# Optimization experiments

Hardware: AMD Instinct MI355X
Metric: run time of the kernel (lower is better)

The kernel has to match this reference:

```python
import jax, jax.numpy as jnp
import numpy as np

B, N, D = 2, 2048, 1024
H = 16                      # num_heads, head_dim = 64
E, K, CF = 4, 2, 1.0        # num_experts, top_k, capacity_factor
MLP_H = int(D * 4.0)        # dense Mlp hidden (mlp_ratio=4.0)
MOE_H = int(D * 0.25)       # expert hidden (hard-coded dim*0.25 in source)


def setup_inputs() -> dict:
    key = jax.random.key(0)
    ks = jax.random.split(key, 12)
    r = lambda k, shp, s=0.02: jax.random.normal(k, shp, jnp.float32) * s
    return dict(
        x=jax.random.normal(ks[0], (B, N, D), jnp.float32),
        noise=jax.random.normal(ks[1], (B, N, E), jnp.float32),
        ln1_g=jnp.ones((D,), jnp.float32), ln1_b=jnp.zeros((D,), jnp.float32),
        ln2_g=jnp.ones((D,), jnp.float32), ln2_b=jnp.zeros((D,), jnp.float32),
        w_qkv=r(ks[2], (3 * D, D)),
        w_proj=r(ks[3], (D, D)), b_proj=jnp.zeros((D,), jnp.float32),
        w_route=r(ks[4], (D, E), 0.05), b_route=jnp.zeros((E,), jnp.float32),
        w_noise=r(ks[5], (D, E), 0.05), b_noise=jnp.zeros((E,), jnp.float32),
        we1=r(ks[6], (E, D, MOE_H)), be1=jnp.zeros((E, MOE_H), jnp.float32),
        we2=r(ks[7], (E, MOE_H, D)), be2=jnp.zeros((E, D), jnp.float32),
        w_mlp1=r(ks[8], (D, MLP_H)), b_mlp1=jnp.zeros((MLP_H,), jnp.float32),
        w_mlp2=r(ks[9], (MLP_H, D)), b_mlp2=jnp.zeros((D,), jnp.float32),
    )


def _ln(x, g, b, eps=1e-5):
    mu = x.mean(-1, keepdims=True)
    var = ((x - mu) ** 2).mean(-1, keepdims=True)
    return (x - mu) * jax.lax.rsqrt(var + eps) * g + b


def _gelu(x):
    return jax.nn.gelu(x, approximate=False)  # torch nn.GELU default (erf)


def reference(x, noise, ln1_g, ln1_b, ln2_g, ln2_b, w_qkv, w_proj, b_proj,
              w_route, b_route, w_noise, b_noise, we1, be1, we2, be2,
              w_mlp1, b_mlp1, w_mlp2, b_mlp2):
    Bs, Ns, Ds = x.shape
    hd = Ds // H
    # --- attention branch ---
    x1 = _ln(x, ln1_g, ln1_b)
    qkv = (x1 @ w_qkv.T).reshape(Bs, Ns, 3, H, hd).transpose(2, 0, 3, 1, 4)
    q, k, v = qkv[0] * (hd ** -0.5), qkv[1], qkv[2]
    attn = jax.nn.softmax(jnp.einsum('bhnd,bhmd->bhnm', q, k), axis=-1)
    ao = jnp.einsum('bhnm,bhmd->bhnd', attn, v).transpose(0, 2, 1, 3).reshape(Bs, Ns, Ds)
    x = x + (ao @ w_proj.T + b_proj)
    # --- shared norm for mlp + moe ---
    x2 = _ln(x, ln2_g, ln2_b)
    # --- noisy top-k router ---
    logits = x2 @ w_route + b_route                  # [B,N,E]
    noisy = logits + noise * jax.nn.softplus(x2 @ w_noise + b_noise)
    topv, topi = jax.lax.top_k(noisy, K)             # [B,N,K]
    probs = jax.nn.softmax(topv, axis=-1)            # softmax over sparse logits == softmax over top-k
    T = Bs * Ns
    flat_x = x2.reshape(T, Ds)
    fidx = topi.reshape(T, K)
    rows = jnp.arange(T)[:, None]
    gate = jnp.zeros((T, E), noisy.dtype).at[rows, fidx].set(probs.reshape(T, K))
    capacity = int(T * K / E * CF)
    # --- capacity-limited dispatch / expert MLP / combine ---
    def dispatch(eid, W1, b1, W2, b2):
        mask = jnp.any(fidx == eid, axis=-1)                     # [T]
        order = jnp.argsort(jnp.logical_not(mask))               # stable: selected tokens first, in token order
        sel = order[:capacity]                                   # [C]
        valid = mask[sel].astype(flat_x.dtype)
        h = _gelu(flat_x[sel] @ W1 + b1)
        out = h @ W2 + b2
        w = gate[sel, eid] * valid
        return sel, out * w[:, None]
    sel, outw = jax.vmap(dispatch)(jnp.arange(E), we1, be1, we2, be2)   # [E,C], [E,C,D]
    moe = jnp.zeros_like(flat_x).at[sel.reshape(-1)].add(outw.reshape(-1, Ds)).reshape(Bs, Ns, Ds)
    # --- dense mlp branch ---
    mlp = _gelu(x2 @ w_mlp1 + b_mlp1) @ w_mlp2 + b_mlp2
    return x + mlp + moe
```

## Files before the change

### kernel.cpp

```cpp
#include <hip/hip_runtime.h>
#include <hip/hip_bf16.h>
#include <math.h>

typedef __bf16 bf16;
typedef __bf16 bf16x4 __attribute__((ext_vector_type(4)));
typedef __bf16 bf16x8 __attribute__((ext_vector_type(8)));
typedef float  f32x4  __attribute__((ext_vector_type(4)));

#define T_TOK 4096
#define DIM   1024
#define NHEAD 16
#define SEQ   2048
#define NEXP  4
#define CAP   2048
#define MLPH  4096
#define MOEH  256

__device__ __forceinline__ float gelu_exact(float v) {
    return 0.5f * v * (1.f + erff(v * 0.70710678118654752f));
}

struct HL { bf16 h, l; };
__device__ __forceinline__ HL split2(float v) {
    HL r; r.h = (bf16)v; r.l = (bf16)(v - (float)r.h); return r;
}

__device__ __forceinline__ float fast_exp2(float x) {
#if __has_builtin(__builtin_amdgcn_exp2f)
    return __builtin_amdgcn_exp2f(x);
#else
    return exp2f(x);
#endif
}

__device__ __forceinline__ void gload16(const bf16* gptr, bf16* lptr) {
    __builtin_amdgcn_global_load_lds(
        (const __attribute__((address_space(1))) unsigned int*)gptr,
        (__attribute__((address_space(3))) unsigned int*)lptr,
        16, 0, 0);
}

__device__ __forceinline__ bf16x8 sw_frag(const bf16* arr, int row, int cc) {
    return *(const bf16x8*)&arr[row * 64 + ((cc ^ (row & 7)) * 8)];
}

__global__ __launch_bounds__(256)
void ln_split_kernel(const float* __restrict__ x, const float* __restrict__ g,
                     const float* __restrict__ b, bf16* __restrict__ oh, bf16* __restrict__ ol) {
    int wave = threadIdx.x >> 6, lane = threadIdx.x & 63;
    long t = (long)blockIdx.x * 4 + wave;
    const float* xr = x + t * DIM;
    float v[16];
    #pragma unroll
    for (int i = 0; i < 16; i++) v[i] = xr[i * 64 + lane];
    float s = 0.f, s2 = 0.f;
    #pragma unroll
    for (int i = 0; i < 16; i++) { s += v[i]; s2 += v[i] * v[i]; }
    #pragma unroll
    for (int m = 1; m < 64; m <<= 1) { s += __shfl_xor(s, m); s2 += __shfl_xor(s2, m); }
    float mu  = s * (1.f / DIM);
    float var = s2 * (1.f / DIM) - mu * mu;
    float rs  = 1.f / sqrtf(var + 1e-5f);
    #pragma unroll
    for (int i = 0; i < 16; i++) {
        int d = i * 64 + lane;
        HL sp = split2((v[i] - mu) * rs * g[d] + b[d]);
        oh[t * DIM + d] = sp.h; ol[t * DIM + d] = sp.l;
    }
}

__global__ __launch_bounds__(256)
void split_pair_kernel(const float* __restrict__ in, bf16* __restrict__ h, bf16* __restrict__ l) {
    long i0 = ((long)blockIdx.x * 256 + threadIdx.x) * 4;
    f32x4 v = *(const f32x4*)&in[i0];
    bf16x4 vh, vl;
    #pragma unroll
    for (int j = 0; j < 4; j++) { HL sp = split2(v[j]); vh[j] = sp.h; vl[j] = sp.l; }
    *(bf16x4*)&h[i0] = vh; *(bf16x4*)&l[i0] = vl;
}

__global__ __launch_bounds__(256)
void transpose_conv_kernel(const float* __restrict__ in, bf16* __restrict__ out, int R, int C) {
    __shared__ bf16 tile[32][33];
    long bo = (long)blockIdx.z * R * C;
    in += bo; out += bo;
    int c0 = blockIdx.x * 32, r0 = blockIdx.y * 32;
    int tx = threadIdx.x & 31, ty = threadIdx.x >> 5;
    #pragma unroll
    for (int i = 0; i < 32; i += 8)
        tile[ty + i][tx] = (bf16)in[(long)(r0 + ty + i) * C + c0 + tx];
    __syncthreads();
    #pragma unroll
    for (int i = 0; i < 32; i += 8)
        out[(long)(c0 + ty + i) * R + r0 + tx] = tile[tx][ty + i];
}

__global__ __launch_bounds__(256)
void gemm_qkv(const bf16* __restrict__ Ah_g, const bf16* __restrict__ Al_g,
              const bf16* __restrict__ Bh_g, const bf16* __restrict__ Bl_g,
              bf16* __restrict__ Qh_g, bf16* __restrict__ Ql_g,
              bf16* __restrict__ Kh_g, bf16* __restrict__ Kl_g,
              bf16* __restrict__ VtI) {
    const int K = DIM;
    __shared__ alignas(16) bf16 Ah[8192], Al[8192], Bh[8192], Bl[8192];
    int tid = threadIdx.x;
    int wave = tid >> 6, lane = tid & 63;
    int l16 = lane & 15, l4 = lane >> 4;
    int wr = (wave >> 1) * 64, wc = (wave & 1) * 64;
    int row0 = blockIdx.y * 128, col0 = blockIdx.x * 128;
    int r8s = lane >> 3;
    int colb = ((lane & 7) ^ r8s) * 8;
    f32x4 acc[4][4] = {};
    for (int k0 = 0; k0 < K; k0 += 64) {
        #pragma unroll
        for (int p = 0; p < 4; p++) {
            int rl = p * 32 + wave * 8 + r8s;
            int lb = p * 2048 + wave * 512;
            gload16(&Ah_g[(long)(row0 + rl) * K + k0 + colb], &Ah[lb]);
            gload16(&Al_g[(long)(row0 + rl) * K + k0 + colb], &Al[lb]);
            gload16(&Bh_g[(long)(col0 + rl) * K + k0 + colb], &Bh[lb]);
            gload16(&Bl_g[(long)(col0 + rl) * K + k0 + colb], &Bl[lb]);
        }
        __syncthreads();
        #pragma unroll
        for (int ks = 0; ks < 2; ks++) {
            bf16x8 ah[4], al[4], bh[4], bl[4];
            #pragma unroll
            for (int i = 0; i < 4; i++) {
                ah[i] = sw_frag(Ah, wr + i*16 + l16, ks*4 + l4);
                al[i] = sw_frag(Al, wr + i*16 + l16, ks*4 + l4);
            }
            #pragma unroll
            for (int j = 0; j < 4; j++) {
                bh[j] = sw_frag(Bh, wc + j*16 + l16, ks*4 + l4);
                bl[j] = sw_frag(Bl, wc + j*16 + l16, ks*4 + l4);
            }
            #pragma unroll
            for (int i = 0; i < 4; i++)
                #pragma unroll
                for (int j = 0; j < 4; j++) {
                    acc[i][j] = __builtin_amdgcn_mfma_f32_16x16x32_bf16(ah[i], bh[j], acc[i][j], 0, 0, 0);
                    acc[i][j] = __builtin_amdgcn_mfma_f32_16x16x32_bf16(ah[i], bl[j], acc[i][j], 0, 0, 0);
                    acc[i][j] = __builtin_amdgcn_mfma_f32_16x16x32_bf16(al[i], bh[j], acc[i][j], 0, 0, 0);
                }
        }
        __syncthreads();
    }
    if (col0 < 2048) {
        bool isQ = (col0 < 1024);
        bf16* oh = isQ ? Qh_g : Kh_g;
        bf16* ol = isQ ? Ql_g : Kl_g;
        float qscale = isQ ? 0.18033688011112043f : 1.0f;
        #pragma unroll
        for (int i = 0; i < 4; i++)
            #pragma unroll
            for (int r = 0; r < 4; r++) {
                int t = row0 + wr + i * 16 + l4 * 4 + r;
                int bq = t >> 11, s = t & 2047;
                #pragma unroll
                for (int j = 0; j < 4; j++) {
                    int col = (col0 + wc + j * 16 + l16) & 1023;
                    int hh = col >> 6, dl = col & 63;
                    long o = ((long)(bq * NHEAD + hh) * SEQ + s) * 64 + dl;
                    HL sp = split2(acc[i][j][r] * qscale);
                    oh[o] = sp.h;
                    if (!isQ) ol[o] = sp.l;
                }
            }
    } else {
        #pragma unroll
        for (int i = 0; i < 4; i++) {
            int s0 = row0 + wr + i * 16 + l4 * 4;
            int b = s0 >> 11, sl = s0 & 2047;
            #pragma unroll
            for (int j = 0; j < 4; j++) {
                int d = col0 - 2048 + wc + j * 16 + l16;
                int h = d >> 6, dl = d & 63;
                long base = ((long)(b * NHEAD + h) * 64 + dl) * (2 * SEQ) + 2 * sl;
                bf16x8 vi;
                #pragma unroll
                for (int r = 0; r < 4; r++) {
                    HL sp = split2(acc[i][j][r]);
                    vi[2 * r] = sp.h; vi[2 * r + 1] = sp.l;
                }
                *(bf16x8*)&VtI[base] = vi;
            }
        }
    }
}

__global__ __launch_bounds__(512, 4)
void flash_attn(const bf16* __restrict__ Qh_g,
                const bf16* __restrict__ Kh_g, const bf16* __restrict__ Kl_g,
                const bf16* __restrict__ VtI_g,
                bf16* __restrict__ aoh, bf16* __restrict__ aol) {
    __shared__ alignas(16) bf16 KhS[2][4096], KlS[2][4096], VIS[2][8192];
    int tid = threadIdx.x;
    int wave = tid >> 6, lane = tid & 63;
    int l16 = lane & 15, l4 = lane >> 4;
    int bid = blockIdx.x;
    int bh = bid & 31;
    int b = bh >> 4, h = bh & 15;
    int q0 = (bid >> 5) * 128;

    bf16x8 qfh[2];
    {
        const bf16* qh = Qh_g + ((long)bh * SEQ + q0 + wave * 16 + l16) * 64;
        #pragma unroll
        for (int ks = 0; ks < 2; ks++)
            qfh[ks] = *(const bf16x8*)&qh[ks * 32 + l4 * 8];
    }
    int r8 = lane >> 3;
    int c8 = lane & 7;
    int r4 = lane >> 4, c16 = lane & 15;
    const bf16* kh_g = Kh_g + (long)bh * SEQ * 64;
    const bf16* kl_g = Kl_g + (long)bh * SEQ * 64;
    const bf16* vI_g = VtI_g + (long)bh * 64 * (2 * SEQ);

    float m_s = -1e30f, l_s = 0.f;
    f32x4 accO[4] = {};

    auto stage = [&](int c0, int bsel) {
        int R0 = wave * 8;
        int row = R0 + r8;
        int ksw = (c8 ^ r8) * 8;
        gload16(&kh_g[(long)(c0 + row) * 64 + ksw], &KhS[bsel][R0 * 64]);
        gload16(&kl_g[(long)(c0 + row) * 64 + ksw], &KlS[bsel][R0 * 64]);
        #pragma unroll
        for (int q = 0; q < 2; q++) {
            int d0 = R0 + q * 4 + r4;
            gload16(&vI_g[(long)d0 * (2 * SEQ) + 2 * c0 + ((c16 ^ (d0 & 15)) * 8)],
                    &VIS[bsel][(R0 + q * 4) * 128]);
        }
    };

    auto compute = [&](const bf16* KhT, const bf16* KlT, const bf16* VIT) {
        f32x4 st[4] = {};
        __builtin_amdgcn_s_setprio(1);
        #pragma unroll
        for (int ks = 0; ks < 2; ks++) {
            #pragma unroll
            for (int i = 0; i < 4; i++) {
                bf16x8 akh = sw_frag(KhT, i * 16 + l16, ks * 4 + l4);
                bf16x8 akl = sw_frag(KlT, i * 16 + l16, ks * 4 + l4);
                st[i] = __builtin_amdgcn_mfma_f32_16x16x32_bf16(akh, qfh[ks], st[i], 0, 0, 0);
                st[i] = __builtin_amdgcn_mfma_f32_16x16x32_bf16(akl, qfh[ks], st[i], 0, 0, 0);
            }
        }
        __builtin_amdgcn_s_setprio(0);
        float mx = st[0][0];
        #pragma unroll
        for (int i = 0; i < 4; i++)
            #pragma unroll
            for (int r = 0; r < 4; r++) mx = fmaxf(mx, st[i][r]);
        mx = fmaxf(mx, __shfl_xor(mx, 16));
        mx = fmaxf(mx, __shfl_xor(mx, 32));
        if (!__all(mx <= m_s + 8.f)) {
            float mnew = fmaxf(m_s, mx);
            float alpha = fast_exp2(m_s - mnew);
            l_s *= alpha;
            #pragma unroll
            for (int i = 0; i < 4; i++)
                #pragma unroll
                for (int r = 0; r < 4; r++) accO[i][r] *= alpha;
            m_s = mnew;
        }
        float psum = 0.f;
        bf16x8 pw[4];
        #pragma unroll
        for (int kb = 0; kb < 4; kb++)
            #pragma unroll
            for (int r = 0; r < 4; r++) {
                float pv = fast_exp2(st[kb][r] - m_s);
                psum += pv;
                bf16 pb = (bf16)pv;
                pw[kb][2 * r] = pb; pw[kb][2 * r + 1] = pb;
            }
        psum += __shfl_xor(psum, 16);
        psum += __shfl_xor(psum, 32);
        l_s += psum;
        __builtin_amdgcn_s_setprio(1);
        #pragma unroll
        for (int kb = 0; kb < 4; kb++) {
            #pragma unroll
            for (int i = 0; i < 4; i++) {
                int d = i * 16 + l16;
                bf16x8 av = *(const bf16x8*)&VIT[d * 128 + (((kb * 4 + l4) ^ (d & 15)) * 8)];
                accO[i] = __builtin_amdgcn_mfma_f32_16x16x32_bf16(av, pw[kb], accO[i], 0, 0, 0);
            }
        }
        __builtin_amdgcn_s_setprio(0);
    };

    const int NT = SEQ / 64;
    stage(0, 0);
    #pragma unroll 1
    for (int t = 0; t < NT; t += 2) {
        stage((t + 1) * 64, 1);
        asm volatile("s_waitcnt vmcnt(4)" ::: "memory");
        __builtin_amdgcn_sched_barrier(0);
        __builtin_amdgcn_s_barrier();
        compute(KhS[0], KlS[0], VIS[0]);
        asm volatile("" ::: "memory");
        __builtin_amdgcn_s_barrier();
        if (t + 2 < NT) {
            stage((t + 2) * 64, 0);
            asm volatile("s_waitcnt vmcnt(4)" ::: "memory");
        } else {
            asm volatile("s_waitcnt vmcnt(0)" ::: "memory");
        }
        __builtin_amdgcn_sched_barrier(0);
        __builtin_amdgcn_s_barrier();
        compute(KhS[1], KlS[1], VIS[1]);
        asm volatile("" ::: "memory");
        __builtin_amdgcn_s_barrier();
    }

    float inv = 1.f / l_s;
    int q = q0 + wave * 16 + l16;
    #pragma unroll
    for (int i = 0; i < 4; i++) {
        bf16x4 oh4, ol4;
        #pragma unroll
        for (int r = 0; r < 4; r++) { HL sp = split2(accO[i][r] * inv); oh4[r] = sp.h; ol4[r] = sp.l; }
        long o = ((long)(b * SEQ + q)) * DIM + h * 64 + i * 16 + l4 * 4;
        *(bf16x4*)&aoh[o] = oh4;
        *(bf16x4*)&aol[o] = ol4;
    }
}

__global__ __launch_bounds__(256)
void gemm_proj(const bf16* __restrict__ Ah_g, const bf16* __restrict__ Al_g,
               const bf16* __restrict__ Bh_g, const bf16* __restrict__ Bl_g,
               const float* __restrict__ bias, const float* __restrict__ res,
               float* __restrict__ C, int N, int K) {
    __shared__ alignas(16) bf16 Ah[8192], Al[8192], Bh[8192], Bl[8192];
    int tid = threadIdx.x;
    int wave = tid >> 6, lane = tid & 63;
    int l16 = lane & 15, l4 = lane >> 4;
    int wr = (wave >> 1) * 64, wc = (wave & 1) * 64;
    int row0 = blockIdx.y * 128, col0 = blockIdx.x * 128;
    int r8s = lane >> 3;
    int colb = ((lane & 7) ^ r8s) * 8;
    f32x4 acc[4][4] = {};
    for (int k0 = 0; k0 < K; k0 += 64) {
        #pragma unroll
        for (int p = 0; p < 4; p++) {
            int rl = p * 32 + wave * 8 + r8s;
            int lb = p * 2048 + wave * 512;
            gload16(&Ah_g[(long)(row0 + rl) * K + k0 + colb], &Ah[lb]);
            gload16(&Al_g[(long)(row0 + rl) * K + k0 + colb], &Al[lb]);
            gload16(&Bh_g[(long)(col0 + rl) * K + k0 + colb], &Bh[lb]);
            gload16(&Bl_g[(long)(col0 + rl) * K + k0 + colb], &Bl[lb]);
        }
        __syncthreads();
        #pragma unroll
        for (int ks = 0; ks < 2; ks++) {
            bf16x8 ah[4], al[4], bh[4], bl[4];
            #pragma unroll
            for (int i = 0; i < 4; i++) {
                ah[i] = sw_frag(Ah, wr + i*16 + l16, ks*4 + l4);
                al[i] = sw_frag(Al, wr + i*16 + l16, ks*4 + l4);
            }
            #pragma unroll
            for (int j = 0; j < 4; j++) {
                bh[j] = sw_frag(Bh, wc + j*16 + l16, ks*4 + l4);
                bl[j] = sw_frag(Bl, wc + j*16 + l16, ks*4 + l4);
            }
            #pragma unroll
            for (int i = 0; i < 4; i++)
                #pragma unroll
                for (int j = 0; j < 4; j++) {
                    acc[i][j] = __builtin_amdgcn_mfma_f32_16x16x32_bf16(ah[i], bh[j], acc[i][j], 0, 0, 0);
                    acc[i][j] = __builtin_amdgcn_mfma_f32_16x16x32_bf16(ah[i], bl[j], acc[i][j], 0, 0, 0);
                    acc[i][j] = __builtin_amdgcn_mfma_f32_16x16x32_bf16(al[i], bh[j], acc[i][j], 0, 0, 0);
                }
        }
        __syncthreads();
    }
    #pragma unroll
    for (int i = 0; i < 4; i++)
        #pragma unroll
        for (int r = 0; r < 4; r++) {
            int grow = row0 + wr + i * 16 + l4 * 4 + r;
            #pragma unroll
            for (int j = 0; j < 4; j++) {
                int gcol = col0 + wc + j * 16 + l16;
                long o = (long)grow * N + gcol;
                C[o] = acc[i][j][r] + bias[gcol] + res[o];
            }
        }
}

template<bool BIAS, bool GELU, bool GATHER, int OUT_MODE>
__global__ __launch_bounds__(256)
void gemm_bt(const bf16* __restrict__ A, const bf16* __restrict__ Bt,
             const float* __restrict__ bias,
             bf16* __restrict__ Cbf, float* __restrict__ Cf,
             const int* __restrict__ rowmap, const float* __restrict__ roww,
             int M, int N, int K,
             long eA, long eB, long ebias, long eMap, long eC) {
    int ez = blockIdx.z;
    A += (long)ez * eA; Bt += (long)ez * eB;
    if (BIAS) bias += (long)ez * ebias;
    if (GATHER || OUT_MODE == 3) rowmap += (long)ez * eMap;
    if (OUT_MODE == 3) roww += (long)ez * eMap;
    if (OUT_MODE == 0) Cbf += (long)ez * eC;

    __shared__ alignas(16) bf16 As[8192];
    __shared__ alignas(16) bf16 Bs[8192];
    int tid = threadIdx.x;
    int wave = tid >> 6, lane = tid & 63;
    int l16 = lane & 15, l4 = lane >> 4;
    int wr = (wave >> 1) * 64, wc = (wave & 1) * 64;
    int row0 = blockIdx.y * 128, col0 = blockIdx.x * 128;
    int r8s = lane >> 3;
    int colb = ((lane & 7) ^ r8s) * 8;

    long arow[4];
    #pragma unroll
    for (int p = 0; p < 4; p++) {
        long gr = row0 + p * 32 + wave * 8 + r8s;
        if (GATHER) gr = rowmap[gr];
        arow[p] = gr;
    }
    f32x4 acc[4][4] = {};
    for (int k0 = 0; k0 < K; k0 += 64) {
        #pragma unroll
        for (int p = 0; p < 4; p++) {
            int rl = p * 32 + wave * 8 + r8s;
            int lb = p * 2048 + wave * 512;
            gload16(&A[arow[p] * K + k0 + colb], &As[lb]);
            gload16(&Bt[(long)(col0 + rl) * K + k0 + colb], &Bs[lb]);
        }
        __syncthreads();
        #pragma unroll
        for (int ks = 0; ks < 2; ks++) {
            bf16x8 af[4], bfr[4];
            #pragma unroll
            for (int i = 0; i < 4; i++) af[i]  = sw_frag(As, wr + i*16 + l16, ks*4 + l4);
            #pragma unroll
            for (int j = 0; j < 4; j++) bfr[j] = sw_frag(Bs, wc + j*16 + l16, ks*4 + l4);
            #pragma unroll
            for (int i = 0; i < 4; i++)
                #pragma unroll
                for (int j = 0; j < 4; j++)
                    acc[i][j] = __builtin_amdgcn_mfma_f32_16x16x32_bf16(af[i], bfr[j], acc[i][j], 0, 0, 0);
        }
        __syncthreads();
    }
    #pragma unroll
    for (int i = 0; i < 4; i++)
        #pragma unroll
        for (int r = 0; r < 4; r++) {
            int grow = row0 + wr + i * 16 + l4 * 4 + r;
            int st = 0; float sw = 0.f;
            if (OUT_MODE == 3) { st = rowmap[grow]; sw = roww[grow]; }
            #pragma unroll
            for (int j = 0; j < 4; j++) {
                int gcol = col0 + wc + j * 16 + l16;
                float v = acc[i][j][r];
                if (BIAS) v += bias[gcol];
                if (GELU) v = gelu_exact(v);
                if (OUT_MODE == 0) {
                    Cbf[(long)grow * N + gcol] = (bf16)v;
                } else if (OUT_MODE == 2) {
                    long o = (long)grow * N + gcol;
                    Cf[o] += v;
                } else {
                    atomicAdd(&Cf[(long)st * N + gcol], sw * v);
                }
            }
        }
}

__global__ __launch_bounds__(256)
void routing_kernel(const float* __restrict__ xres, const float* __restrict__ g,
                    const float* __restrict__ b, const float* __restrict__ w_route,
                    const float* __restrict__ b_route, const float* __restrict__ w_noise,
                    const float* __restrict__ b_noise, const float* __restrict__ noise,
                    int* __restrict__ topi, float* __restrict__ topp,
                    bf16* __restrict__ x2b) {
    int wave = threadIdx.x >> 6, lane = threadIdx.x & 63;
    long t = (long)blockIdx.x * 4 + wave;
    const float* xr = xres + t * DIM;
    float v[16];
    #pragma unroll
    for (int i = 0; i < 16; i++) v[i] = xr[i * 64 + lane];
    float s = 0.f, s2 = 0.f;
    #pragma unroll
    for (int i = 0; i < 16; i++) { s += v[i]; s2 += v[i] * v[i]; }
    #pragma unroll
    for (int m = 1; m < 64; m <<= 1) { s += __shfl_xor(s, m); s2 += __shfl_xor(s2, m); }
    float mu  = s * (1.f / DIM);
    float var = s2 * (1.f / DIM) - mu * mu;
    float rs  = 1.f / sqrtf(var + 1e-5f);
    float accr[4] = {0.f,0.f,0.f,0.f}, accn[4] = {0.f,0.f,0.f,0.f};
    #pragma unroll
    for (int i = 0; i < 16; i++) {
        int d = i * 64 + lane;
        float n = (v[i] - mu) * rs * g[d] + b[d];
        x2b[t * DIM + d] = (bf16)n;
        #pragma unroll
        for (int e = 0; e < 4; e++) {
            accr[e] += n * w_route[d * 4 + e];
            accn[e] += n * w_noise[d * 4 + e];
        }
    }
    #pragma unroll
    for (int e = 0; e < 4; e++)
        #pragma unroll
        for (int m = 1; m < 64; m <<= 1) {
            accr[e] += __shfl_xor(accr[e], m);
            accn[e] += __shfl_xor(accn[e], m);
        }
    if (lane == 0) {
        float nz[4];
        #pragma unroll
        for (int e = 0; e < 4; e++) {
            float logit = accr[e] + b_route[e];
            float si = accn[e] + b_noise[e];
            float sp = si > 0.f ? si + log1pf(expf(-si)) : log1pf(expf(si));
            nz[e] = logit + noise[t * 4 + e] * sp;
        }
        int i1 = 0;
        #pragma unroll
        for (int e = 1; e < 4; e++) if (nz[e] > nz[i1]) i1 = e;
        int i2 = -1; float v2 = -1e30f;
        #pragma unroll
        for (int e = 0; e < 4; e++) if (e != i1 && nz[e] > v2) { v2 = nz[e]; i2 = e; }
        float ex = expf(v2 - nz[i1]);
        topi[t * 2]     = i1; topi[t * 2 + 1] = i2;
        topp[t * 2]     = 1.f / (1.f + ex);
        topp[t * 2 + 1] = ex / (1.f + ex);
    }
}

__global__ __launch_bounds__(256)
void dispatch_kernel(const int* __restrict__ topi, const float* __restrict__ topp,
                     int* __restrict__ sel, float* __restrict__ wgt) {
    int e = threadIdx.x >> 6, lane = threadIdx.x & 63;
    int cnt = 0;
    for (int c = 0; c < T_TOK; c += 64) {
        int t = c + lane;
        int i0 = topi[t * 2], i1 = topi[t * 2 + 1];
        bool m = (i0 == e) || (i1 == e);
        unsigned long long bal = __ballot(m);
        int pos = cnt + __popcll(bal & ((1ull << lane) - 1ull));
        if (m && pos < CAP) {
            sel[e * CAP + pos] = t;
            wgt[e * CAP + pos] = (i0 == e) ? topp[t * 2] : topp[t * 2 + 1];
        }
        cnt += (int)__popcll(bal);
    }
    if (cnt > CAP) cnt = CAP;
    for (int pos = cnt + lane; pos < CAP; pos += 64) {
        sel[e * CAP + pos] = 0;
        wgt[e * CAP + pos] = 0.f;
    }
}

extern "C" void kernel_launch(void* const* d_in, const int* in_sizes, int n_in,
                              void* d_out, int out_size, void* d_ws, size_t ws_size,
                              hipStream_t stream) {
    (void)in_sizes; (void)n_in; (void)out_size; (void)ws_size;
    const float* x       = (const float*)d_in[0];
    const float* noise   = (const float*)d_in[1];
    const float* ln1_g   = (const float*)d_in[2];
    const float* ln1_b   = (const float*)d_in[3];
    const float* ln2_g   = (const float*)d_in[4];
    const float* ln2_b   = (const float*)d_in[5];
    const float* w_qkv   = (const float*)d_in[6];
    const float* w_proj  = (const float*)d_in[7];
    const float* b_proj  = (const float*)d_in[8];
    const float* w_route = (const float*)d_in[9];
    const float* b_route = (const float*)d_in[10];
    const float* w_noise = (const float*)d_in[11];
    const float* b_noise = (const float*)d_in[12];
    const float* we1     = (const float*)d_in[13];
    const float* be1     = (const float*)d_in[14];
    const float* we2     = (const float*)d_in[15];
    const float* be2     = (const float*)d_in[16];
    const float* w_mlp1  = (const float*)d_in[17];
    const float* b_mlp1  = (const float*)d_in[18];
    const float* w_mlp2  = (const float*)d_in[19];
    const float* b_mlp2  = (const float*)d_in[20];
    float* d_outf = (float*)d_out;

    const size_t MB = 1024 * 1024;
    char* ws = (char*)d_ws;
    bf16* x1h = (bf16*)(ws);
    bf16* x1l = (bf16*)(ws + 8 * MB);
    bf16* aoh = (bf16*)(ws);
    bf16* aol = (bf16*)(ws + 8 * MB);
    bf16* w_mlp1T = (bf16*)(ws);
    bf16* w_mlp2T = (bf16*)(ws + 8 * MB);
    bf16* wqkvh = (bf16*)(ws + 16 * MB);
    bf16* wqkvl = (bf16*)(ws + 22 * MB);
    bf16* we1T  = (bf16*)(ws + 16 * MB);
    bf16* we2T  = (bf16*)(ws + 18 * MB);
    bf16* h_e   = (bf16*)(ws + 20 * MB);
    bf16* wprojh = (bf16*)(ws + 28 * MB);
    bf16* wprojl = (bf16*)(ws + 30 * MB);
    bf16* Qh = (bf16*)(ws + 32 * MB);
    bf16* Ql = (bf16*)(ws + 40 * MB);
    bf16* Kh = (bf16*)(ws + 48 * MB);
    bf16* Kl = (bf16*)(ws + 56 * MB);
    bf16* h_mlp = (bf16*)(ws + 32 * MB);
    bf16*  VtI  = (bf16*)(ws + 64 * MB);
    bf16*  x2b  = (bf16*)(ws + 64 * MB);
    int*   topi = (int*)(ws + 72 * MB);
    float* topp = (float*)(ws + 72 * MB + 32768);
    int*   sel  = (int*)(ws + 72 * MB + 65536);
    float* wgt  = (float*)(ws + 72 * MB + 98304);

    ln_split_kernel<<<T_TOK/4, 256, 0, stream>>>(x, ln1_g, ln1_b, x1h, x1l);
    split_pair_kernel<<<(3*DIM*DIM)/1024, 256, 0, stream>>>(w_qkv, wqkvh, wqkvl);
    split_pair_kernel<<<(DIM*DIM)/1024,   256, 0, stream>>>(w_proj, wprojh, wprojl);

    gemm_qkv<<<dim3(3*DIM/128, T_TOK/128), 256, 0, stream>>>(
        x1h, x1l, wqkvh, wqkvl, Qh, Ql, Kh, Kl, VtI);

    flash_attn<<<dim3(32 * (SEQ/128)), 512, 0, stream>>>(Qh, Kh, Kl, VtI, aoh, aol);

    gemm_proj<<<dim3(DIM/128, T_TOK/128), 256, 0, stream>>>(
        aoh, aol, wprojh, wprojl, b_proj, x, d_outf, DIM, DIM);

    routing_kernel<<<T_TOK/4, 256, 0, stream>>>(d_outf, ln2_g, ln2_b, w_route, b_route,
                                                w_noise, b_noise, noise, topi, topp, x2b);
    dispatch_kernel<<<1, 256, 0, stream>>>(topi, topp, sel, wgt);

    transpose_conv_kernel<<<dim3(MLPH/32, DIM/32, 1),    256, 0, stream>>>(w_mlp1, w_mlp1T, DIM, MLPH);
    transpose_conv_kernel<<<dim3(DIM/32, MLPH/32, 1),    256, 0, stream>>>(w_mlp2, w_mlp2T, MLPH, DIM);
    transpose_conv_kernel<<<dim3(MOEH/32, DIM/32, NEXP), 256, 0, stream>>>(we1, we1T, DIM, MOEH);
    transpose_conv_kernel<<<dim3(DIM/32, MOEH/32, NEXP), 256, 0, stream>>>(we2, we2T, MOEH, DIM);

    gemm_bt<true,true,false,0><<<dim3(MLPH/128, T_TOK/128), 256, 0, stream>>>(
        x2b, w_mlp1T, b_mlp1, h_mlp, nullptr, nullptr, nullptr, T_TOK, MLPH, DIM,
        0, 0, 0, 0, 0);
    gemm_bt<true,false,false,2><<<dim3(DIM/128, T_TOK/128), 256, 0, stream>>>(
        h_mlp, w_mlp2T, b_mlp2, nullptr, d_outf, nullptr, nullptr, T_TOK, DIM, MLPH,
        0, 0, 0, 0, 0);

    gemm_bt<true,true,true,0><<<dim3(MOEH/128, CAP/128, NEXP), 256, 0, stream>>>(
        x2b, we1T, be1, h_e, nullptr, sel, nullptr, CAP, MOEH, DIM,
        0, (long)MOEH*DIM, MOEH, CAP, (long)CAP*MOEH);
    gemm_bt<true,false,false,3><<<dim3(DIM/128, CAP/128, NEXP), 256, 0, stream>>>(
        h_e, we2T, be2, nullptr, d_outf, sel, wgt, CAP, DIM, MOEH,
        (long)CAP*MOEH, (long)DIM*MOEH, DIM, CAP, 0);
}
```

Baseline: 622.5 us.

## Add XCD-aware tile swizzle and split-K atomic reduction for MLP down-projection

Adds an XCD-aware remapping of workgroup ids so that neighbouring output tiles land on the same chiplet, applied to the QKV, projection and generic GEMMs to improve L2 reuse. The MLP second GEMM (K=4096, only 256 tiles) is split four ways along K across blockIdx.z. Each slice atomically adds its partial sum into the fp32 output, and only the first slice adds the bias. This raises parallelism on the long-K GEMM at the cost of extra atomic traffic and a nondeterministic summation order.

```diff
diff --git a/kernel.cpp b/kernel.cpp
--- a/kernel.cpp
+++ b/kernel.cpp
@@ -42,6 +42,16 @@
 
 __device__ __forceinline__ bf16x8 sw_frag(const bf16* arr, int row, int cc) {
     return *(const bf16x8*)&arr[row * 64 + ((cc ^ (row & 7)) * 8)];
+}
+
+__device__ __forceinline__ void xcd_tile(int& bx, int& by) {
+    int gx = gridDim.x;
+    int nwg = gx * gridDim.y;
+    int flat = blockIdx.y * gx + blockIdx.x;
+    int q = nwg >> 3, r = nwg & 7;
+    int xcd = flat & 7, loc = flat >> 3;
+    int swz = (xcd < r ? xcd * (q + 1) : r * (q + 1) + (xcd - r) * q) + loc;
+    bx = swz % gx; by = swz / gx;
 }
 
 __global__ __launch_bounds__(256)
@@ -107,7 +117,8 @@
     int wave = tid >> 6, lane = tid & 63;
     int l16 = lane & 15, l4 = lane >> 4;
     int wr = (wave >> 1) * 64, wc = (wave & 1) * 64;
-    int row0 = blockIdx.y * 128, col0 = blockIdx.x * 128;
+    int bx, by; xcd_tile(bx, by);
+    int row0 = by * 128, col0 = bx * 128;
     int r8s = lane >> 3;
     int colb = ((lane & 7) ^ r8s) * 8;
     f32x4 acc[4][4] = {};
@@ -339,7 +350,8 @@
     int wave = tid >> 6, lane = tid & 63;
     int l16 = lane & 15, l4 = lane >> 4;
     int wr = (wave >> 1) * 64, wc = (wave & 1) * 64;
-    int row0 = blockIdx.y * 128, col0 = blockIdx.x * 128;
+    int bx, by; xcd_tile(bx, by);
+    int row0 = by * 128, col0 = bx * 128;
     int r8s = lane >> 3;
     int colb = ((lane & 7) ^ r8s) * 8;
     f32x4 acc[4][4] = {};
@@ -392,7 +404,7 @@
         }
 }
 
-template<bool BIAS, bool GELU, bool GATHER, int OUT_MODE>
+template<bool BIAS, bool GELU, bool GATHER, int OUT_MODE, int SPLITK = 1>
 __global__ __launch_bounds__(256)
 void gemm_bt(const bf16* __restrict__ A, const bf16* __restrict__ Bt,
              const float* __restrict__ bias,
@@ -401,11 +413,16 @@
              int M, int N, int K,
              long eA, long eB, long ebias, long eMap, long eC) {
     int ez = blockIdx.z;
-    A += (long)ez * eA; Bt += (long)ez * eB;
-    if (BIAS) bias += (long)ez * ebias;
-    if (GATHER || OUT_MODE == 3) rowmap += (long)ez * eMap;
-    if (OUT_MODE == 3) roww += (long)ez * eMap;
-    if (OUT_MODE == 0) Cbf += (long)ez * eC;
+    int kbase = 0;
+    if (SPLITK > 1) {
+        kbase = ez * (K / SPLITK);
+    } else {
+        A += (long)ez * eA; Bt += (long)ez * eB;
+        if (BIAS) bias += (long)ez * ebias;
+        if (GATHER || OUT_MODE == 3) rowmap += (long)ez * eMap;
+        if (OUT_MODE == 3) roww += (long)ez * eMap;
+        if (OUT_MODE == 0) Cbf += (long)ez * eC;
+    }
 
     __shared__ alignas(16) bf16 As[8192];
     __shared__ alignas(16) bf16 Bs[8192];
@@ -413,7 +430,8 @@
     int wave = tid >> 6, lane = tid & 63;
     int l16 = lane & 15, l4 = lane >> 4;
     int wr = (wave >> 1) * 64, wc = (wave & 1) * 64;
-    int row0 = blockIdx.y * 128, col0 = blockIdx.x * 128;
+    int bx, by; xcd_tile(bx, by);
+    int row0 = by * 128, col0 = bx * 128;
     int r8s = lane >> 3;
     int colb = ((lane & 7) ^ r8s) * 8;
 
@@ -424,14 +442,15 @@
         if (GATHER) gr = rowmap[gr];
         arow[p] = gr;
     }
+    const int KC = (SPLITK > 1) ? (K / SPLITK) : K;
     f32x4 acc[4][4] = {};
-    for (int k0 = 0; k0 < K; k0 += 64) {
+    for (int k0 = 0; k0 < KC; k0 += 64) {
         #pragma unroll
         for (int p = 0; p < 4; p++) {
             int rl = p * 32 + wave * 8 + r8s;
             int lb = p * 2048 + wave * 512;
-            gload16(&A[arow[p] * K + k0 + colb], &As[lb]);
-            gload16(&Bt[(long)(col0 + rl) * K + k0 + colb], &Bs[lb]);
+            gload16(&A[arow[p] * K + kbase + k0 + colb], &As[lb]);
+            gload16(&Bt[(long)(col0 + rl) * K + kbase + k0 + colb], &Bs[lb]);
         }
         __syncthreads();
         #pragma unroll
@@ -460,6 +479,12 @@
             for (int j = 0; j < 4; j++) {
                 int gcol = col0 + wc + j * 16 + l16;
                 float v = acc[i][j][r];
+                if (OUT_MODE == 4) {
+                    if (BIAS && ez == 0) v += bias[gcol];
+                    if (GELU) v = gelu_exact(v);
+                    atomicAdd(&Cf[(long)grow * N + gcol], v);
+                    continue;
+                }
                 if (BIAS) v += bias[gcol];
                 if (GELU) v = gelu_exact(v);
                 if (OUT_MODE == 0) {
@@ -638,7 +663,7 @@
     gemm_bt<true,true,false,0><<<dim3(MLPH/128, T_TOK/128), 256, 0, stream>>>(
         x2b, w_mlp1T, b_mlp1, h_mlp, nullptr, nullptr, nullptr, T_TOK, MLPH, DIM,
         0, 0, 0, 0, 0);
-    gemm_bt<true,false,false,2><<<dim3(DIM/128, T_TOK/128), 256, 0, stream>>>(
+    gemm_bt<true,false,false,4,4><<<dim3(DIM/128, T_TOK/128, 4), 256, 0, stream>>>(
         h_mlp, w_mlp2T, b_mlp2, nullptr, d_outf, nullptr, nullptr, T_TOK, DIM, MLPH,
         0, 0, 0, 0, 0);
 
```

Measured after the change: 624.8 us. No clear change (+0.4%).
